# Kernel optimization log

Measured on AMD Instinct MI355X. Metric: run time of the kernel, lower is better.

Reference implementation:

```python
import jax, jax.numpy as jnp
import numpy as np

N = 160000
K = 16
C_IN = 64
C_OUT = 128
C_MID = 16  # weightnet out


def _lin_bn(x, W, g, b):
    # Linear (no bias) followed by eval-mode BatchNorm folded into per-channel affine
    return (x @ W) * g + b


def _lrelu(x):
    return jnp.where(x > 0, x, 0.1 * x)


def setup_inputs() -> dict:
    key = jax.random.key(0)
    ks = jax.random.split(key, 12)
    d = {}
    d['dense_xyz'] = jax.random.normal(ks[0], (1, N, 3), dtype=jnp.float32)
    d['dense_feats'] = jax.random.normal(ks[1], (1, N, C_IN), dtype=jnp.float32)
    d['nei_inds'] = jax.random.randint(ks[2], (1, N, K), 0, N, dtype=jnp.int32)
    def lin(k, fan_in, fan_out):
        return jax.random.normal(k, (fan_in, fan_out), dtype=jnp.float32) / np.sqrt(fan_in)
    d['W_u1'] = lin(ks[3], C_IN, C_OUT // 4)
    d['g_u1'] = jnp.ones((C_OUT // 4,), jnp.float32); d['b_u1'] = jnp.zeros((C_OUT // 4,), jnp.float32)
    d['W_wn0'] = lin(ks[4], 3, 8); d['g_wn0'] = jnp.ones((8,), jnp.float32); d['b_wn0'] = jnp.zeros((8,), jnp.float32)
    d['W_wn1'] = lin(ks[5], 8, 8); d['g_wn1'] = jnp.ones((8,), jnp.float32); d['b_wn1'] = jnp.zeros((8,), jnp.float32)
    d['W_wn2'] = lin(ks[6], 8, C_MID); d['g_wn2'] = jnp.ones((C_MID,), jnp.float32); d['b_wn2'] = jnp.zeros((C_MID,), jnp.float32)
    d['W_lin'] = lin(ks[7], (C_OUT // 4) * C_MID, C_OUT // 2)
    d['g_lin'] = jnp.ones((C_OUT // 2,), jnp.float32); d['b_lin'] = jnp.zeros((C_OUT // 2,), jnp.float32)
    d['W_u2'] = lin(ks[8], C_OUT // 2, C_OUT)
    d['g_u2'] = jnp.ones((C_OUT,), jnp.float32); d['b_u2'] = jnp.zeros((C_OUT,), jnp.float32)
    d['W_sc'] = lin(ks[9], C_IN, C_OUT)
    d['g_sc'] = jnp.ones((C_OUT,), jnp.float32); d['b_sc'] = jnp.zeros((C_OUT,), jnp.float32)
    return d


def reference(dense_xyz, dense_feats, nei_inds,
              W_u1, g_u1, b_u1,
              W_wn0, g_wn0, b_wn0,
              W_wn1, g_wn1, b_wn1,
              W_wn2, g_wn2, b_wn2,
              W_lin, g_lin, b_lin,
              W_u2, g_u2, b_u2,
              W_sc, g_sc, b_sc):
    B, n, _ = dense_xyz.shape
    gather = jax.vmap(lambda tbl, idx: tbl[idx])  # (n,c),(n,k)->(n,k,c), vmapped over batch

    # unary1: Linear+BN+LeakyReLU(0.1)
    feats_x = _lrelu(_lin_bn(dense_feats, W_u1, g_u1, b_u1))  # [B,N,32]

    gathered_xyz = gather(dense_xyz, nei_inds)                 # [B,N,K,3]
    localized_xyz = gathered_xyz - dense_xyz[:, :, None, :]    # [B,N,K,3]

    w = jax.nn.relu(_lin_bn(localized_xyz, W_wn0, g_wn0, b_wn0))
    w = jax.nn.relu(_lin_bn(w, W_wn1, g_wn1, b_wn1))
    w = jax.nn.relu(_lin_bn(w, W_wn2, g_wn2, b_wn2))           # [B,N,K,16]

    gathered_feat = gather(feats_x, nei_inds)                  # [B,N,K,32]
    # PointConv aggregation: per-point (C x K) @ (K x C_mid)
    new_feat = jnp.einsum('bnkc,bnkw->bncw', gathered_feat, w).reshape(B, n, -1)  # [B,N,512]

    new_feat = jax.nn.relu(_lin_bn(new_feat, W_lin, g_lin, b_lin))  # [B,N,64]
    new_feat = _lin_bn(new_feat, W_u2, g_u2, b_u2)                  # [B,N,128], no relu

    shortcut = _lin_bn(dense_feats, W_sc, g_sc, b_sc)               # [B,N,128]
    out = _lrelu(new_feat + shortcut)
    return out, localized_xyz
```

## Files before the change

kernel.cpp:

```cpp
#include <hip/hip_runtime.h>
#include <stdint.h>

typedef unsigned short u16;
typedef unsigned int   u32;

typedef __attribute__((ext_vector_type(8))) short bf16x8;
typedef __attribute__((ext_vector_type(4))) float f32x4;


__device__ __forceinline__ float bf2f(u16 h) {
  return __uint_as_float(((u32)h) << 16);
}
__device__ __forceinline__ float lrelu(float x) { return x > 0.f ? x : 0.1f * x; }

__device__ __forceinline__ float ldf(const void* p, size_t i, bool bf) {
  return bf ? bf2f(((const u16*)p)[i]) : ((const float*)p)[i];
}
__device__ __forceinline__ bool probe_bf16(const void* g) {
  return ((*(const u32*)g) & 0xFFFFu) == 0x3F80u;
}
__device__ __forceinline__ u16 f2bf(float x) {
  u32 u = __float_as_uint(x);
  return (u16)((u + 0x7FFFu + ((u >> 16) & 1u)) >> 16);
}

__global__ __launch_bounds__(256) void k1_unary(
    const void* __restrict__ feats, const void* __restrict__ W,
    const void* __restrict__ g, const void* __restrict__ b,
    float* __restrict__ fx, int Npts)
{
  __shared__ float sW[64 * 32];
  __shared__ float sb[32];
  __shared__ float sf[8][64];
  bool bf = probe_bf16(g);
  int tid = threadIdx.x;
  for (int e = tid; e < 2048; e += 256) sW[e] = ldf(W, e, bf) * ldf(g, e & 31, bf);
  if (tid < 32) sb[tid] = ldf(b, tid, bf);
  int n0 = blockIdx.x * 8;
  for (int e = tid; e < 512; e += 256) {
    int p = e >> 6, i = e & 63;
    int n = n0 + p;
    sf[p][i] = (n < Npts) ? ldf(feats, (size_t)n * 64 + i, bf) : 0.f;
  }
  __syncthreads();
  int p = tid >> 5, c = tid & 31;
  int n = n0 + p;
  if (n < Npts) {
    float acc = sb[c];
#pragma unroll
    for (int i = 0; i < 64; ++i) acc += sf[p][i] * sW[i * 32 + c];
    fx[(size_t)n * 32 + c] = lrelu(acc);
  }
}

__global__ __launch_bounds__(256) void k2_point(
    const void* __restrict__ xyz, const int* __restrict__ nei,
    const float* __restrict__ fx,
    const void* __restrict__ W0, const void* __restrict__ g0, const void* __restrict__ b0,
    const void* __restrict__ W1, const void* __restrict__ g1, const void* __restrict__ b1,
    const void* __restrict__ W2, const void* __restrict__ g2, const void* __restrict__ b2,
    u16* __restrict__ nf16, float* __restrict__ locout, int n0, int n1)
{
  __shared__ float sW0[24], sB0[8], sW1[64], sB1[8], sW2[128], sB2[16];
  __shared__ int   sIdx[4][16];
  __shared__ float sLoc[4][48];
  __shared__ float sHa[4][128];
  __shared__ float sHb[4][128];
  alignas(16) __shared__ float sP[4][256];
  alignas(16) __shared__ float sGF[4][512];

  bool bf = probe_bf16(g0);
  int tid = threadIdx.x;
  if (tid < 24) sW0[tid] = ldf(W0, tid, bf) * ldf(g0, tid & 7, bf);
  else if (tid < 32) sB0[tid - 24] = ldf(b0, tid - 24, bf);
  else if (tid < 96) sW1[tid - 32] = ldf(W1, tid - 32, bf) * ldf(g1, (tid - 32) & 7, bf);
  else if (tid < 104) sB1[tid - 96] = ldf(b1, tid - 96, bf);
  else if (tid < 232) sW2[tid - 104] = ldf(W2, tid - 104, bf) * ldf(g2, (tid - 104) & 15, bf);
  else if (tid < 248) sB2[tid - 232] = ldf(b2, tid - 232, bf);

  int w = tid >> 6, lane = tid & 63;
  int n = n0 + blockIdx.x * 4 + w;
  bool valid = n < n1;

  if (lane < 16) sIdx[w][lane] = valid ? nei[(size_t)n * 16 + lane] : 0;
  __syncthreads();

  if (lane < 48) {
    int k = lane / 3, d = lane - k * 3;
    float v = 0.f;
    if (valid) {
      int m = sIdx[w][k];
      v = ldf(xyz, (size_t)m * 3 + d, bf) - ldf(xyz, (size_t)n * 3 + d, bf);
      locout[(size_t)n * 48 + lane] = v;
    }
    sLoc[w][lane] = v;
  }
  __syncthreads();

#pragma unroll
  for (int r = 0; r < 2; ++r) {
    int o = lane + r * 64;
    int k = o >> 3, j = o & 7;
    float a = sB0[j];
#pragma unroll
    for (int d = 0; d < 3; ++d) a += sLoc[w][k * 3 + d] * sW0[d * 8 + j];
    sHa[w][o] = fmaxf(a, 0.f);
  }
  __syncthreads();
#pragma unroll
  for (int r = 0; r < 2; ++r) {
    int o = lane + r * 64;
    int k = o >> 3, j = o & 7;
    float a = sB1[j];
#pragma unroll
    for (int d = 0; d < 8; ++d) a += sHa[w][k * 8 + d] * sW1[d * 8 + j];
    sHb[w][o] = fmaxf(a, 0.f);
  }
  __syncthreads();
#pragma unroll
  for (int r = 0; r < 4; ++r) {
    int o = lane + r * 64;
    int k = o >> 4, j = o & 15;
    float a = sB2[j];
#pragma unroll
    for (int d = 0; d < 8; ++d) a += sHb[w][k * 8 + d] * sW2[d * 16 + j];
    sP[w][o] = fmaxf(a, 0.f);
  }

  {
    int e0 = lane * 8;
    int k = e0 >> 5, c0 = e0 & 31;
    float4 v0 = make_float4(0.f, 0.f, 0.f, 0.f), v1 = v0;
    if (valid) {
      int m = sIdx[w][k];
      const float4* src = reinterpret_cast<const float4*>(fx + (size_t)m * 32 + c0);
      v0 = src[0]; v1 = src[1];
    }
    float4* dst = reinterpret_cast<float4*>(&sGF[w][e0]);
    dst[0] = v0; dst[1] = v1;
  }
  __syncthreads();

  {
    int c = lane >> 1, mb = (lane & 1) * 8;
    float acc[8] = {0.f, 0.f, 0.f, 0.f, 0.f, 0.f, 0.f, 0.f};
#pragma unroll
    for (int k = 0; k < 16; ++k) {
      float f = sGF[w][k * 32 + c];
      const float4* pw = reinterpret_cast<const float4*>(&sP[w][k * 16 + mb]);
      float4 w0 = pw[0], w1 = pw[1];
      acc[0] += f * w0.x; acc[1] += f * w0.y; acc[2] += f * w0.z; acc[3] += f * w0.w;
      acc[4] += f * w1.x; acc[5] += f * w1.y; acc[6] += f * w1.z; acc[7] += f * w1.w;
    }
    if (valid) {
      bf16x8 pk;
#pragma unroll
      for (int e = 0; e < 8; ++e) pk[e] = (short)f2bf(acc[e]);
      *reinterpret_cast<bf16x8*>(nf16 + (size_t)(n - n0) * 512 + (c * 16 + mb)) = pk;
    }
  }
}

__global__ __launch_bounds__(256) void k3_gemm(
    const u16* __restrict__ nf, const void* __restrict__ WL,
    const void* __restrict__ gl, const void* __restrict__ bl,
    u16* __restrict__ h, int cnt)
{
  alignas(16) __shared__ u16 As[128 * 64];
  alignas(16) __shared__ u16 Bs[64 * 512];
  bool bf = probe_bf16(gl);
  int t = threadIdx.x;
  int lane = t & 63, w = t >> 6;
  int m0 = blockIdx.x * 128;

  {
    int c = t & 63, kh = t >> 6;
    float gc = ldf(gl, c, bf);
    int k0 = kh * 128;
#pragma unroll
    for (int q = 0; q < 16; ++q) {
      int kbase = k0 + q * 8;
      bf16x8 pk;
#pragma unroll
      for (int e = 0; e < 8; ++e)
        pk[e] = (short)f2bf(ldf(WL, (size_t)(kbase + e) * 64 + c, bf) * gc);
      int chunk = (kbase >> 3) ^ (c & 7);
      *reinterpret_cast<bf16x8*>(&Bs[c * 512 + chunk * 8]) = pk;
    }
  }

  f32x4 acc[2][4];
#pragma unroll
  for (int mi = 0; mi < 2; ++mi)
#pragma unroll
    for (int ni = 0; ni < 4; ++ni) acc[mi][ni] = (f32x4){0.f, 0.f, 0.f, 0.f};

  int mrow = t >> 1;
  int half = t & 1;

  for (int kb = 0; kb < 512; kb += 64) {
    __syncthreads();
    {
      int gm = m0 + mrow;
      if (gm >= cnt) gm = cnt - 1;
      const u16* src = nf + (size_t)gm * 512 + kb + half * 32;
#pragma unroll
      for (int q = 0; q < 4; ++q) {
        bf16x8 v = *reinterpret_cast<const bf16x8*>(src + q * 8);
        int chunk = (half * 4 + q) ^ (mrow & 7);
        *reinterpret_cast<bf16x8*>(&As[mrow * 64 + chunk * 8]) = v;
      }
    }
    __syncthreads();
#pragma unroll
    for (int ks = 0; ks < 2; ++ks) {
      int qg = lane >> 4;
      bf16x8 a[2];
#pragma unroll
      for (int mi = 0; mi < 2; ++mi) {
        int row = w * 32 + mi * 16 + (lane & 15);
        int chunk = (ks * 4 + qg) ^ (row & 7);
        a[mi] = *reinterpret_cast<const bf16x8*>(&As[row * 64 + chunk * 8]);
      }
      bf16x8 bfr[4];
#pragma unroll
      for (int ni = 0; ni < 4; ++ni) {
        int col = ni * 16 + (lane & 15);
        int chunk = ((kb >> 3) + ks * 4 + qg) ^ (col & 7);
        bfr[ni] = *reinterpret_cast<const bf16x8*>(&Bs[col * 512 + chunk * 8]);
      }
#pragma unroll
      for (int mi = 0; mi < 2; ++mi)
#pragma unroll
        for (int ni = 0; ni < 4; ++ni)
          acc[mi][ni] = __builtin_amdgcn_mfma_f32_16x16x32_bf16(
              a[mi], bfr[ni], acc[mi][ni], 0, 0, 0);
    }
  }

  int colb = lane & 15, rq = lane >> 4;
  float bias[4];
#pragma unroll
  for (int ni = 0; ni < 4; ++ni) bias[ni] = ldf(bl, ni * 16 + colb, bf);
#pragma unroll
  for (int mi = 0; mi < 2; ++mi) {
#pragma unroll
    for (int v = 0; v < 4; ++v) {
      int m = m0 + w * 32 + mi * 16 + rq * 4 + v;
      if (m < cnt) {
#pragma unroll
        for (int ni = 0; ni < 4; ++ni) {
          int j = ni * 16 + colb;
          h[(size_t)m * 64 + j] = f2bf(fmaxf(acc[mi][ni][v] + bias[ni], 0.f));
        }
      }
    }
  }
}

__global__ __launch_bounds__(256) void k4_gemm(
    const u16* __restrict__ hb, const void* __restrict__ feats,
    const void* __restrict__ Wu2, const void* __restrict__ gu2, const void* __restrict__ bu2,
    const void* __restrict__ Wsc, const void* __restrict__ gsc, const void* __restrict__ bsc,
    float* __restrict__ out, int n0c, int cnt)
{
  alignas(16) __shared__ u16 As[128 * 128];
  alignas(16) __shared__ u16 Bs[128 * 128];
  bool bf = probe_bf16(gu2);
  int t = threadIdx.x;
  int lane = t & 63, w = t >> 6;
  int m0 = blockIdx.x * 128;

  {
    int c = t & 127, kh = t >> 7;
    const void* Wsel = kh ? Wsc : Wu2;
    const void* gsel = kh ? gsc : gu2;
    float gc = ldf(gsel, c, bf);
#pragma unroll
    for (int q = 0; q < 8; ++q) {
      bf16x8 pk;
#pragma unroll
      for (int e = 0; e < 8; ++e)
        pk[e] = (short)f2bf(ldf(Wsel, (size_t)(q * 8 + e) * 128 + c, bf) * gc);
      int chunk = (kh * 8 + q) ^ (c & 7);
      *reinterpret_cast<bf16x8*>(&Bs[c * 128 + chunk * 8]) = pk;
    }
  }
  {
    int r = t >> 1, half = t & 1;
    int gm = m0 + r;
    if (gm >= cnt) gm = cnt - 1;
    if (half == 0) {
      const u16* src = hb + (size_t)gm * 64;
#pragma unroll
      for (int q = 0; q < 8; ++q) {
        bf16x8 v = *reinterpret_cast<const bf16x8*>(src + q * 8);
        int chunk = q ^ (r & 7);
        *reinterpret_cast<bf16x8*>(&As[r * 128 + chunk * 8]) = v;
      }
    } else if (bf) {
      const u16* src = (const u16*)feats + (size_t)(n0c + gm) * 64;
#pragma unroll
      for (int q = 0; q < 8; ++q) {
        bf16x8 v = *reinterpret_cast<const bf16x8*>(src + q * 8);
        int chunk = (8 + q) ^ (r & 7);
        *reinterpret_cast<bf16x8*>(&As[r * 128 + chunk * 8]) = v;
      }
    } else {
      const float* src = (const float*)feats + (size_t)(n0c + gm) * 64;
#pragma unroll
      for (int q = 0; q < 8; ++q) {
        bf16x8 pk;
#pragma unroll
        for (int e = 0; e < 8; ++e) pk[e] = (short)f2bf(src[q * 8 + e]);
        int chunk = (8 + q) ^ (r & 7);
        *reinterpret_cast<bf16x8*>(&As[r * 128 + chunk * 8]) = pk;
      }
    }
  }
  __syncthreads();

  f32x4 acc[2][8];
#pragma unroll
  for (int mi = 0; mi < 2; ++mi)
#pragma unroll
    for (int ni = 0; ni < 8; ++ni) acc[mi][ni] = (f32x4){0.f, 0.f, 0.f, 0.f};

  int qg = lane >> 4;
#pragma unroll
  for (int ks = 0; ks < 4; ++ks) {
    bf16x8 a[2];
#pragma unroll
    for (int mi = 0; mi < 2; ++mi) {
      int row = w * 32 + mi * 16 + (lane & 15);
      int chunk = (ks * 4 + qg) ^ (row & 7);
      a[mi] = *reinterpret_cast<const bf16x8*>(&As[row * 128 + chunk * 8]);
    }
#pragma unroll
    for (int ni = 0; ni < 8; ++ni) {
      int col = ni * 16 + (lane & 15);
      int chunk = (ks * 4 + qg) ^ (col & 7);
      bf16x8 b = *reinterpret_cast<const bf16x8*>(&Bs[col * 128 + chunk * 8]);
      acc[0][ni] = __builtin_amdgcn_mfma_f32_16x16x32_bf16(a[0], b, acc[0][ni], 0, 0, 0);
      acc[1][ni] = __builtin_amdgcn_mfma_f32_16x16x32_bf16(a[1], b, acc[1][ni], 0, 0, 0);
    }
  }

  int colb = lane & 15, rq = lane >> 4;
  float bias[8];
#pragma unroll
  for (int ni = 0; ni < 8; ++ni) {
    int c = ni * 16 + colb;
    bias[ni] = ldf(bu2, c, bf) + ldf(bsc, c, bf);
  }
#pragma unroll
  for (int mi = 0; mi < 2; ++mi) {
#pragma unroll
    for (int v = 0; v < 4; ++v) {
      int m = m0 + w * 32 + mi * 16 + rq * 4 + v;
      if (m < cnt) {
        float* orow = out + (size_t)(n0c + m) * 128;
#pragma unroll
        for (int ni = 0; ni < 8; ++ni)
          orow[ni * 16 + colb] = lrelu(acc[mi][ni][v] + bias[ni]);
      }
    }
  }
}

extern "C" void kernel_launch(void* const* d_in, const int* in_sizes, int n_in,
                              void* d_out, int out_size, void* d_ws, size_t ws_size,
                              hipStream_t stream) {
  const void* xyz   = d_in[0];
  const void* feats = d_in[1];
  const int*  nei   = (const int*)d_in[2];
  const void* W_u1  = d_in[3];
  const void* g_u1  = d_in[4];
  const void* b_u1  = d_in[5];
  const void* W_wn0 = d_in[6];
  const void* g_wn0 = d_in[7];
  const void* b_wn0 = d_in[8];
  const void* W_wn1 = d_in[9];
  const void* g_wn1 = d_in[10];
  const void* b_wn1 = d_in[11];
  const void* W_wn2 = d_in[12];
  const void* g_wn2 = d_in[13];
  const void* b_wn2 = d_in[14];
  const void* W_lin = d_in[15];
  const void* g_lin = d_in[16];
  const void* b_lin = d_in[17];
  const void* W_u2  = d_in[18];
  const void* g_u2  = d_in[19];
  const void* b_u2  = d_in[20];
  const void* W_sc  = d_in[21];
  const void* g_sc  = d_in[22];
  const void* b_sc  = d_in[23];

  int Npts = in_sizes[0] / 3;

  float* out0 = (float*)d_out;
  float* out1 = out0 + (size_t)Npts * 128;

  float* fx = (float*)d_ws;
  size_t fx_bytes = (size_t)Npts * 32 * 4;
  size_t avail = (ws_size > fx_bytes) ? (ws_size - fx_bytes) : 0;
  size_t per_pt = (size_t)512 * 2 + (size_t)64 * 2;
  long long cN = (long long)(avail / per_pt);
  if (cN < 1) cN = 1;
  if (cN > Npts) cN = Npts;
  int chunkN = (int)cN;

  u16* nf16 = (u16*)(fx + (size_t)Npts * 32);
  u16* hb   = nf16 + (size_t)chunkN * 512;

  k1_unary<<<(Npts + 7) / 8, 256, 0, stream>>>(feats, W_u1, g_u1, b_u1, fx, Npts);

  for (int n0 = 0; n0 < Npts; n0 += chunkN) {
    int n1 = n0 + chunkN;
    if (n1 > Npts) n1 = Npts;
    int cnt = n1 - n0;
    k2_point<<<(cnt + 3) / 4, 256, 0, stream>>>(
        xyz, nei, fx,
        W_wn0, g_wn0, b_wn0, W_wn1, g_wn1, b_wn1, W_wn2, g_wn2, b_wn2,
        nf16, out1, n0, n1);
    k3_gemm<<<(cnt + 127) / 128, 256, 0, stream>>>(nf16, W_lin, g_lin, b_lin, hb, cnt);
    k4_gemm<<<(cnt + 127) / 128, 256, 0, stream>>>(hb, feats, W_u2, g_u2, b_u2,
                                                   W_sc, g_sc, b_sc, out0, n0, cnt);
  }
}
```

Before: 457.8 us.

## Store unary features as bf16 and aggregate neighbors with MFMA

The unary1 output is now stored as bf16, which halves the workspace traffic of the random neighbor gather. The per-point K×C by K×C_mid aggregation now runs as two 16x16x32 bf16 MFMA instructions per wave, reading transposed, padded bf16 tiles in shared memory instead of scalar FMA loops. Only half the lanes feed nonzero data because K=16 is zero-padded to 32. The change adds bf16 rounding of both the gathered features and the weightnet outputs before the aggregation, and the output stores become scattered 2-byte writes instead of 16-byte vector stores.

```diff
diff --git a/kernel.cpp b/kernel.cpp
--- a/kernel.cpp
+++ b/kernel.cpp
@@ -27,7 +27,7 @@
 __global__ __launch_bounds__(256) void k1_unary(
     const void* __restrict__ feats, const void* __restrict__ W,
     const void* __restrict__ g, const void* __restrict__ b,
-    float* __restrict__ fx, int Npts)
+    u16* __restrict__ fx, int Npts)
 {
   __shared__ float sW[64 * 32];
   __shared__ float sb[32];
@@ -49,13 +49,13 @@
     float acc = sb[c];
 #pragma unroll
     for (int i = 0; i < 64; ++i) acc += sf[p][i] * sW[i * 32 + c];
-    fx[(size_t)n * 32 + c] = lrelu(acc);
+    fx[(size_t)n * 32 + c] = f2bf(lrelu(acc));
   }
 }
 
 __global__ __launch_bounds__(256) void k2_point(
     const void* __restrict__ xyz, const int* __restrict__ nei,
-    const float* __restrict__ fx,
+    const u16* __restrict__ fx,
     const void* __restrict__ W0, const void* __restrict__ g0, const void* __restrict__ b0,
     const void* __restrict__ W1, const void* __restrict__ g1, const void* __restrict__ b1,
     const void* __restrict__ W2, const void* __restrict__ g2, const void* __restrict__ b2,
@@ -66,8 +66,8 @@
   __shared__ float sLoc[4][48];
   __shared__ float sHa[4][128];
   __shared__ float sHb[4][128];
-  alignas(16) __shared__ float sP[4][256];
-  alignas(16) __shared__ float sGF[4][512];
+  alignas(16) __shared__ u16 sPT[4][16 * 24];
+  alignas(16) __shared__ u16 sGFT[4][32 * 24];
 
   bool bf = probe_bf16(g0);
   int tid = threadIdx.x;
@@ -95,6 +95,15 @@
     }
     sLoc[w][lane] = v;
   }
+
+  {
+    int k = lane & 15, cg = lane >> 4;
+    int m = sIdx[w][k];
+    bf16x8 v = *reinterpret_cast<const bf16x8*>(fx + (size_t)m * 32 + cg * 8);
+#pragma unroll
+    for (int e = 0; e < 8; ++e)
+      sGFT[w][(cg * 8 + e) * 24 + k] = (u16)v[e];
+  }
   __syncthreads();
 
 #pragma unroll
@@ -124,39 +133,34 @@
     float a = sB2[j];
 #pragma unroll
     for (int d = 0; d < 8; ++d) a += sHb[w][k * 8 + d] * sW2[d * 16 + j];
-    sP[w][o] = fmaxf(a, 0.f);
-  }
+    sPT[w][j * 24 + k] = f2bf(fmaxf(a, 0.f));
+  }
+  __syncthreads();
 
   {
-    int e0 = lane * 8;
-    int k = e0 >> 5, c0 = e0 & 31;
-    float4 v0 = make_float4(0.f, 0.f, 0.f, 0.f), v1 = v0;
+    int kgrp = lane >> 4;
+    int cb = lane & 15;
+    bf16x8 a0 = (bf16x8){0,0,0,0,0,0,0,0};
+    bf16x8 a1 = a0, b = a0;
+    if (kgrp < 2) {
+      a0 = *reinterpret_cast<const bf16x8*>(&sGFT[w][(cb)      * 24 + kgrp * 8]);
+      a1 = *reinterpret_cast<const bf16x8*>(&sGFT[w][(16 + cb) * 24 + kgrp * 8]);
+      b  = *reinterpret_cast<const bf16x8*>(&sPT [w][(cb)      * 24 + kgrp * 8]);
+    }
+    f32x4 acc0 = (f32x4){0.f, 0.f, 0.f, 0.f};
+    f32x4 acc1 = acc0;
+    acc0 = __builtin_amdgcn_mfma_f32_16x16x32_bf16(a0, b, acc0, 0, 0, 0);
+    acc1 = __builtin_amdgcn_mfma_f32_16x16x32_bf16(a1, b, acc1, 0, 0, 0);
     if (valid) {
-      int m = sIdx[w][k];
-      const float4* src = reinterpret_cast<const float4*>(fx + (size_t)m * 32 + c0);
-      v0 = src[0]; v1 = src[1];
-    }
-    float4* dst = reinterpret_cast<float4*>(&sGF[w][e0]);
-    dst[0] = v0; dst[1] = v1;
-  }
-  __syncthreads();
-
-  {
-    int c = lane >> 1, mb = (lane & 1) * 8;
-    float acc[8] = {0.f, 0.f, 0.f, 0.f, 0.f, 0.f, 0.f, 0.f};
-#pragma unroll
-    for (int k = 0; k < 16; ++k) {
-      float f = sGF[w][k * 32 + c];
-      const float4* pw = reinterpret_cast<const float4*>(&sP[w][k * 16 + mb]);
-      float4 w0 = pw[0], w1 = pw[1];
-      acc[0] += f * w0.x; acc[1] += f * w0.y; acc[2] += f * w0.z; acc[3] += f * w0.w;
-      acc[4] += f * w1.x; acc[5] += f * w1.y; acc[6] += f * w1.z; acc[7] += f * w1.w;
-    }
-    if (valid) {
-      bf16x8 pk;
-#pragma unroll
-      for (int e = 0; e < 8; ++e) pk[e] = (short)f2bf(acc[e]);
-      *reinterpret_cast<bf16x8*>(nf16 + (size_t)(n - n0) * 512 + (c * 16 + mb)) = pk;
+      u16* dst = nf16 + (size_t)(n - n0) * 512;
+      int rq = lane >> 4;
+#pragma unroll
+      for (int v = 0; v < 4; ++v) {
+        int c0 = rq * 4 + v;
+        int c1 = 16 + rq * 4 + v;
+        dst[c0 * 16 + cb] = f2bf(acc0[v]);
+        dst[c1 * 16 + cb] = f2bf(acc1[v]);
+      }
     }
   }
 }
@@ -401,8 +405,8 @@
   float* out0 = (float*)d_out;
   float* out1 = out0 + (size_t)Npts * 128;
 
-  float* fx = (float*)d_ws;
-  size_t fx_bytes = (size_t)Npts * 32 * 4;
+  u16* fx = (u16*)d_ws;
+  size_t fx_bytes = (size_t)Npts * 32 * 2;
   size_t avail = (ws_size > fx_bytes) ? (ws_size - fx_bytes) : 0;
   size_t per_pt = (size_t)512 * 2 + (size_t)64 * 2;
   long long cN = (long long)(avail / per_pt);
@@ -410,7 +414,7 @@
   if (cN > Npts) cN = Npts;
   int chunkN = (int)cN;
 
-  u16* nf16 = (u16*)(fx + (size_t)Npts * 32);
+  u16* nf16 = fx + (size_t)Npts * 32;
   u16* hb   = nf16 + (size_t)chunkN * 512;
 
   k1_unary<<<(Npts + 7) / 8, 256, 0, stream>>>(feats, W_u1, g_u1, b_u1, fx, Npts);
```

After: 444.1 us. -3.0%, faster.
